# Kernel tuning notes

Hardware: AMD Instinct MI355X
Metric: run time of the kernel (lower is better)

Reference implementation:

```python
import jax, jax.numpy as jnp
import numpy as np

B, N, C, K = 8, 49104, 90, 1000  # batch, anchors, classes, pre-NMS top-k cap
NEG = -1e9


def _decode(reg, anc):
    # anchors ltrb -> cxcywh, apply reg, back to ltrb (matches decode_boxes)
    l, t, r, b = anc[..., 0], anc[..., 1], anc[..., 2], anc[..., 3]
    w_a, h_a = r - l, b - t
    cx_a, cy_a = l + w_a / 2, t + h_a / 2
    cx = cx_a + reg[..., 0] * w_a
    cy = cy_a + reg[..., 1] * h_a
    w = w_a * jnp.exp(reg[..., 2])
    h = h_a * jnp.exp(reg[..., 3])
    left, top = cx - w / 2, cy - h / 2
    return jnp.stack([left, top, left + w, top + h], -1)


def _iou(boxes):  # [K,4] -> [K,K]
    area = (boxes[:, 2] - boxes[:, 0]) * (boxes[:, 3] - boxes[:, 1])
    lt = jnp.maximum(boxes[:, None, :2], boxes[None, :, :2])
    rb = jnp.minimum(boxes[:, None, 2:], boxes[None, :, 2:])
    wh = jnp.clip(rb - lt, 0.0)
    inter = wh[..., 0] * wh[..., 1]
    return inter / (area[:, None] + area[None, :] - inter + 1e-9)


def _per_image(cls, reg, anchors, size, size_ori, score_thresh, nms_thresh):
    scores = jnp.max(cls, axis=-1)                       # [N]
    labels = jnp.argmax(cls, axis=-1).astype(jnp.int32)  # [N]
    valid = scores >= score_thresh
    boxes = _decode(reg, anchors)                        # [N,4] ltrb
    H = size[0].astype(jnp.float32)
    W = size[1].astype(jnp.float32)
    x = jnp.clip(boxes[..., 0::2], 0.0, W - 1.0)
    y = jnp.clip(boxes[..., 1::2], 0.0, H - 1.0)
    boxes = jnp.stack([x[..., 0], y[..., 0], x[..., 1], y[..., 1]], -1)
    # fixed-size substitute for nonzero(): take top-K by masked score
    ms = jnp.where(valid, scores, NEG)
    top_s, idx = jax.lax.top_k(ms, K)
    b, l, v = boxes[idx], labels[idx], valid[idx]        # [K,4],[K],[K]
    # batched_nms trick: offset boxes per class so classes never overlap
    off = l.astype(jnp.float32) * (jnp.maximum(W, H) + 1.0)
    iou = _iou(b + off[:, None])                         # [K,K]
    ar = jnp.arange(K)
    def body(i, supp):
        keep_i = v[i] & jnp.logical_not(supp[i])
        return supp | (keep_i & (iou[i] > nms_thresh) & (ar > i))
    supp = jax.lax.fori_loop(0, K, body, jnp.zeros((K,), bool))
    keep = v & jnp.logical_not(supp)
    scale = size_ori[0].astype(jnp.float32) / H
    b = b * scale
    out5 = jnp.concatenate(
        [jnp.where(keep[:, None], b, 0.0), jnp.where(keep, top_s, 0.0)[:, None]], -1)
    return out5, jnp.where(keep, l, -1), keep


def setup_inputs() -> dict:
    key = jax.random.key(0)
    k1, k2, k3, k4, k5, k6 = jax.random.split(key, 6)
    classifications = jax.random.uniform(k1, (B, N, C), dtype=jnp.float32)
    regressions = jax.random.normal(k2, (B, N, 4), dtype=jnp.float32) * 0.1
    cx = jax.random.uniform(k3, (N,), minval=0.0, maxval=512.0)
    cy = jax.random.uniform(k4, (N,), minval=0.0, maxval=512.0)
    w = jax.random.uniform(k5, (N,), minval=16.0, maxval=256.0)
    h = jax.random.uniform(k6, (N,), minval=16.0, maxval=256.0)
    anchors = jnp.stack([cx - w / 2, cy - h / 2, cx + w / 2, cy + h / 2], -1)
    return {
        'classifications': classifications,
        'regressions': regressions,
        'anchors': anchors,
        'image_sizes': jnp.full((B, 2), 512, dtype=jnp.int32),
        'image_sizes_ori': jnp.full((B, 2), 768, dtype=jnp.int32),
        'score_thresh': jnp.float32(0.999),
        'nms_thresh': jnp.float32(0.5),
    }


def reference(classifications, regressions, anchors, image_sizes, image_sizes_ori, score_thresh, nms_thresh):
    out5, labels, keep = jax.vmap(
        _per_image, in_axes=(0, 0, None, 0, 0, None, None))(
        classifications, regressions, anchors, image_sizes, image_sizes_ori,
        score_thresh, nms_thresh)
    return out5, labels, keep
```

## Files before the change

kernel.cpp:

```cpp
#include <hip/hip_runtime.h>
#include <stdint.h>

#define NB 8
#define NN 49104
#define NC 90
#define NK 1000
#define SA 192
#define NSEG 256
#define CAP2 8192
#define NB2 4352
#define NB2P 5120

typedef unsigned long long u64;

__global__ __launch_bounds__(768) void k_score(const float* __restrict__ cls,
                                               const float* __restrict__ thr_p,
                                               u64* __restrict__ cseg,
                                               unsigned* __restrict__ segcnt) {
  __shared__ __align__(16) float lds[SA * NC];
  __shared__ unsigned scnt;
  int b = blockIdx.y;
  int blk = blockIdx.x;
  int t0 = blk * SA;
  int tid = threadIdx.x;
  int lane = tid & 63;
  if (tid == 0) scnt = 0u;
  int acnt = NN - t0; if (acnt > SA) acnt = SA;
  const float4* src = (const float4*)(cls + ((size_t)b * NN + t0) * NC);
  float4* dst = (float4*)lds;
  int elems4 = acnt * NC / 4;
  for (int t = tid; t < elems4; t += 768) dst[t] = src[t];
  __syncthreads();
  int a = tid >> 2, q = tid & 3;
  float best = -1e30f; int bc = 0;
  if (a < acnt) {
    for (int c = q; c < NC; c += 4) {
      float v = lds[a * NC + c];
      if (v > best) { best = v; bc = c; }
    }
    float ov; int oc;
    ov = __shfl_xor(best, 1); oc = __shfl_xor(bc, 1);
    if (ov > best || (ov == best && oc < bc)) { best = ov; bc = oc; }
    ov = __shfl_xor(best, 2); oc = __shfl_xor(bc, 2);
    if (ov > best || (ov == best && oc < bc)) { best = ov; bc = oc; }
  }
  bool valid = (q == 0) && (a < acnt) && (best >= *thr_p);
  u64 key = 0ULL;
  if (valid) {
    unsigned idx = (unsigned)(t0 + a);
    key = ((u64)__float_as_uint(best) << 32) |
          ((u64)(0xFFFFu - idx) << 16) | (u64)(unsigned)bc;
  }
  __syncthreads();
  u64* kbuf = (u64*)lds;
  u64 m = __ballot(valid);
  if (m) {
    int leader = (int)__ffsll((unsigned long long)m) - 1;
    unsigned base = 0;
    if (lane == leader) base = atomicAdd(&scnt, (unsigned)__popcll(m));
    base = __shfl(base, leader);
    if (valid) {
      unsigned pos = base + (unsigned)__popcll(m & ((1ULL << lane) - 1ULL));
      kbuf[pos] = key;
    }
  }
  __syncthreads();
  unsigned cnt = scnt;
  u64* dseg = cseg + ((size_t)b * NSEG + blk) * SA;
  for (unsigned t = tid; t < cnt; t += 768) dseg[t] = kbuf[t];
  if (tid == 0) segcnt[b * NSEG + blk] = cnt;
}

__device__ __forceinline__ void decode_box(const float4 rg, const float4 an,
                                           float W, float H, float* out) {
#pragma clang fp contract(off)
  float l = an.x, t = an.y, r = an.z, bo = an.w;
  float wa = r - l, ha = bo - t;
  float cxa = l + wa * 0.5f, cya = t + ha * 0.5f;
  float cx = cxa + rg.x * wa;
  float cy = cya + rg.y * ha;
  float w = wa * expf(rg.z);
  float h = ha * expf(rg.w);
  float left = cx - w * 0.5f, top = cy - h * 0.5f;
  float right = left + w, botm = top + h;
  out[0] = fminf(fmaxf(left, 0.f), W - 1.f);
  out[1] = fminf(fmaxf(top, 0.f), H - 1.f);
  out[2] = fminf(fmaxf(right, 0.f), W - 1.f);
  out[3] = fminf(fmaxf(botm, 0.f), H - 1.f);
}

__global__ __launch_bounds__(1024) void k_worker(
    const u64* __restrict__ cseg, const unsigned* __restrict__ segcnt,
    const float* __restrict__ regs, const float* __restrict__ anch,
    const int* __restrict__ isz, const int* __restrict__ iszo,
    const float* __restrict__ nthr_p, float* __restrict__ out) {
#pragma clang fp contract(off)
  __shared__ __align__(16) char S[151552];
  __shared__ unsigned wsum[16];
  __shared__ unsigned segc[NSEG];
  __shared__ unsigned sofsL[NSEG + 1];
  __shared__ unsigned wcar[4];
  __shared__ int lcnt[NC];
  __shared__ int lofs[NC + 1];

  u64* cand = (u64*)S;
  u64* outk = (u64*)(S + 65536);
  unsigned* hist = (unsigned*)(S + 131072);

  int tid = threadIdx.x;
  int lane = tid & 63, wid = tid >> 6;
  int b = blockIdx.x;

  for (int i = tid; i < NB2P; i += 1024) hist[i] = 0u;
  if (tid < NSEG) {
    unsigned c = segcnt[b * NSEG + tid]; if (c > SA) c = SA;
    segc[tid] = c;
  }
  __syncthreads();

  unsigned vv = 0;
  if (tid < NSEG) {
    vv = segc[tid];
    for (int d = 1; d < 64; d <<= 1) {
      unsigned o = __shfl_up(vv, d);
      if (lane >= d) vv += o;
    }
    if (lane == 63) wcar[wid] = vv;
  }
  __syncthreads();
  if (tid < NSEG) {
    unsigned add = 0;
    for (int w = 0; w < wid; w++) add += wcar[w];
    sofsL[tid] = add + vv - segc[tid];
    if (tid == NSEG - 1) sofsL[NSEG] = add + vv;
  }
  __syncthreads();
  unsigned total = sofsL[NSEG]; if (total > CAP2) total = CAP2;

  {
    int s = tid >> 2, sub = tid & 3;
    unsigned c = segc[s], o = sofsL[s];
    const u64* srcp = cseg + ((size_t)b * NSEG + s) * SA;
    for (unsigned j = sub; j < c; j += 4) {
      u64 key = srcp[j];
      unsigned pos = o + j;
      if (pos < CAP2) {
        cand[pos] = key;
        unsigned bin = (0x3F800000u - (unsigned)(key >> 32) - 1u) >> 2;
        if (bin >= NB2) bin = NB2 - 1;
        atomicAdd(&hist[bin], 1u);
      }
    }
  }
  __syncthreads();

  int base5 = tid * 5;
  unsigned mysum = 0;
#pragma unroll
  for (int i = 0; i < 5; i++) mysum += hist[base5 + i];
  unsigned v = mysum;
  for (int d = 1; d < 64; d <<= 1) {
    unsigned o = __shfl_up(v, d);
    if (lane >= d) v += o;
  }
  if (lane == 63) wsum[wid] = v;
  __syncthreads();
  if (tid == 0) {
    unsigned acc = 0;
    for (int w2 = 0; w2 < 16; w2++) { unsigned c = wsum[w2]; wsum[w2] = acc; acc += c; }
  }
  __syncthreads();
  unsigned running = wsum[wid] + v - mysum;
#pragma unroll
  for (int i = 0; i < 5; i++) {
    unsigned c = hist[base5 + i];
    hist[base5 + i] = running;
    running += c;
  }
  __syncthreads();

  for (unsigned p = tid; p < total; p += 1024) {
    u64 key = cand[p];
    unsigned bin = (0x3F800000u - (unsigned)(key >> 32) - 1u) >> 2;
    if (bin >= NB2) bin = NB2 - 1;
    unsigned pos = atomicAdd(&hist[bin], 1u);
    if (pos < CAP2) outk[pos] = key;
  }
  __syncthreads();

  for (int bin = tid; bin < NB2; bin += 1024) {
    unsigned hi = hist[bin];
    unsigned lo = bin ? hist[bin - 1] : 0u;
    if (hi > CAP2) hi = CAP2;
    if (lo > CAP2) lo = CAP2;
    if (hi > lo + 1) {
      for (unsigned i2 = lo + 1; i2 < hi; i2++) {
        u64 kx = outk[i2];
        int j = (int)i2 - 1;
        while (j >= (int)lo && outk[j] < kx) { outk[j + 1] = outk[j]; j--; }
        outk[j + 1] = kx;
      }
    }
  }
  __syncthreads();

  int n = (int)total; if (n > NK) n = NK;
  float4* bo = (float4*)S;
  unsigned short* llab = (unsigned short*)(S + 16000);
  unsigned short* sidx = (unsigned short*)(S + 18000);
  unsigned char* live = (unsigned char*)(S + 20000);
  u64* clsbits = (u64*)(S + 21008);
  u64* nmsmask = (u64*)(S + 32536);

  float H = (float)isz[b * 2 + 0];
  float W = (float)isz[b * 2 + 1];
  float scale = (float)iszo[b * 2 + 0] / H;
  float offmul = fmaxf(W, H) + 1.0f;
  for (int i = tid; i < NC * 16; i += 1024) clsbits[i] = 0ULL;
  for (int k = tid; k < n; k += 1024) {
    u64 key = outk[k];
    float sc = __uint_as_float((unsigned)(key >> 32));
    unsigned idx = 0xFFFFu - (unsigned)((key >> 16) & 0xFFFFull);
    int lab = (int)(key & 0xFFFFull);
    float raw[4];
    float4 rg = ((const float4*)regs)[(size_t)b * NN + idx];
    float4 an = ((const float4*)anch)[idx];
    decode_box(rg, an, W, H, raw);
    float off = (float)lab * offmul;
    bo[k] = make_float4(raw[0] + off, raw[1] + off, raw[2] + off, raw[3] + off);
    llab[k] = (unsigned short)lab;
    live[k] = 1;
    int g = b * NK + k;
    float* o5 = out + (size_t)g * 5;
    o5[0] = raw[0] * scale; o5[1] = raw[1] * scale;
    o5[2] = raw[2] * scale; o5[3] = raw[3] * scale;
    o5[4] = sc;
    out[(size_t)NB * NK * 5 + g] = (float)lab;
  }
  __syncthreads();

  for (int k = tid; k < n; k += 1024)
    atomicOr(&clsbits[(int)llab[k] * 16 + (k >> 6)], 1ULL << (k & 63));
  __syncthreads();

  if (tid < NC) {
    unsigned cnt = 0;
#pragma unroll
    for (int w = 0; w < 16; w++) cnt += (unsigned)__popcll(clsbits[tid * 16 + w]);
    lcnt[tid] = (int)cnt;
  }
  __syncthreads();
  if (tid == 0) {
    int acc = 0;
    for (int c = 0; c < NC; c++) { lofs[c] = acc; acc += lcnt[c]; }
    lofs[NC] = acc;
  }
  __syncthreads();

  for (int k = tid; k < n; k += 1024) {
    int lab = (int)llab[k];
    const u64* cb = &clsbits[lab * 16];
    int w0 = k >> 6;
    unsigned pos = 0;
    for (int w = 0; w < w0; w++) pos += (unsigned)__popcll(cb[w]);
    pos += (unsigned)__popcll(cb[w0] & ((1ULL << (k & 63)) - 1ULL));
    sidx[lofs[lab] + pos] = (unsigned short)k;
  }
  __syncthreads();

  float thr = *nthr_p;
  for (int p = tid; p < n; p += 1024) {
    int ki = (int)sidx[p];
    int lab = (int)llab[ki];
    int s = lofs[lab], e = lofs[lab + 1];
    int r = p - s;
    if (r < 64) {
      u64 mask = 0ULL;
      float4 Bb = bo[ki];
      float x0 = Bb.x, y0 = Bb.y, x1 = Bb.z, y1 = Bb.w;
      float ai = (x1 - x0) * (y1 - y0);
      int qe = e; if (qe > s + 64) qe = s + 64;
      for (int q = p + 1; q < qe; q++) {
        int kj = (int)sidx[q];
        float4 Cc = bo[kj];
        float aj = (Cc.z - Cc.x) * (Cc.w - Cc.y);
        float ltx = fmaxf(x0, Cc.x), lty = fmaxf(y0, Cc.y);
        float rbx = fminf(x1, Cc.z), rby = fminf(y1, Cc.w);
        float ww = fmaxf(rbx - ltx, 0.f), hh = fmaxf(rby - lty, 0.f);
        float inter = ww * hh;
        float den = ((ai + aj) - inter) + 1e-9f;
        float iou = inter / den;
        if (iou > thr) mask |= 1ULL << (q - s);
      }
      nmsmask[lab * 64 + r] = mask;
    }
  }
  __syncthreads();

  if (tid < NC) {
    int s = lofs[tid], e = lofs[tid + 1], m = e - s;
    if (m <= 64) {
      u64 rem = 0ULL;
      for (int r = 0; r < m; r++)
        if (!((rem >> r) & 1ULL)) rem |= nmsmask[tid * 64 + r];
      for (int r = 0; r < m; r++)
        live[(int)sidx[s + r]] = (unsigned char)(1ULL ^ ((rem >> r) & 1ULL));
    } else {
      for (int r = 0; r < m; r++) live[(int)sidx[s + r]] = 1;
      for (int i = s; i < e; i++) {
        int ki = (int)sidx[i];
        if (!live[ki]) continue;
        float4 Bb = bo[ki];
        float x0 = Bb.x, y0 = Bb.y, x1 = Bb.z, y1 = Bb.w;
        float ai = (x1 - x0) * (y1 - y0);
        for (int j = i + 1; j < e; j++) {
          int kj = (int)sidx[j];
          if (!live[kj]) continue;
          float4 Cc = bo[kj];
          float aj = (Cc.z - Cc.x) * (Cc.w - Cc.y);
          float ltx = fmaxf(x0, Cc.x), lty = fmaxf(y0, Cc.y);
          float rbx = fminf(x1, Cc.z), rby = fminf(y1, Cc.w);
          float ww = fmaxf(rbx - ltx, 0.f), hh = fmaxf(rby - lty, 0.f);
          float inter = ww * hh;
          float den = ((ai + aj) - inter) + 1e-9f;
          float iou = inter / den;
          if (iou > thr) live[kj] = 0;
        }
      }
    }
  }
  __syncthreads();

  for (int k = tid; k < NK; k += 1024) {
    int g = b * NK + k;
    int keep = (k < n) ? (int)live[k] : 0;
    if (keep) {
      out[(size_t)NB * NK * 6 + g] = 1.0f;
    } else {
      float* o5 = out + (size_t)g * 5;
      o5[0] = 0.f; o5[1] = 0.f; o5[2] = 0.f; o5[3] = 0.f; o5[4] = 0.f;
      out[(size_t)NB * NK * 5 + g] = -1.0f;
      out[(size_t)NB * NK * 6 + g] = 0.0f;
    }
  }
}

extern "C" void kernel_launch(void* const* d_in, const int* in_sizes, int n_in,
                              void* d_out, int out_size, void* d_ws, size_t ws_size,
                              hipStream_t stream) {
  const float* cls = (const float*)d_in[0];
  const float* regs = (const float*)d_in[1];
  const float* anch = (const float*)d_in[2];
  const int* isz = (const int*)d_in[3];
  const int* iszo = (const int*)d_in[4];
  const float* sthr = (const float*)d_in[5];
  const float* nthr = (const float*)d_in[6];
  float* out = (float*)d_out;

  char* p = (char*)d_ws;
  auto alloc = [&](size_t bytes) {
    char* r = p;
    p += (bytes + 255) & ~(size_t)255;
    return r;
  };
  u64* cseg = (u64*)alloc((size_t)NB * NSEG * SA * 8);
  unsigned* segcnt = (unsigned*)alloc((size_t)NB * NSEG * 4);

  hipLaunchKernelGGL(k_score, dim3(NSEG, NB), dim3(768), 0, stream,
                     cls, sthr, cseg, segcnt);
  hipLaunchKernelGGL(k_worker, dim3(NB), dim3(1024), 0, stream,
                     cseg, segcnt, regs, anch, isz, iszo, nthr, out);
}
```

Before: 55.59 us.

## Fuse score and worker kernels into one persistent launch with atomic completion counters

```diff
diff --git a/kernel.cpp b/kernel.cpp
--- a/kernel.cpp
+++ b/kernel.cpp
@@ -7,68 +7,25 @@
 #define NK 1000
 #define SA 192
 #define NSEG 256
-#define CAP2 8192
+#define NTH 768
+#define CAP 6912
 #define NB2 4352
-#define NB2P 5120
+#define HISTN 5376
+#define NWORK 8
 
 typedef unsigned long long u64;
 
-__global__ __launch_bounds__(768) void k_score(const float* __restrict__ cls,
-                                               const float* __restrict__ thr_p,
-                                               u64* __restrict__ cseg,
-                                               unsigned* __restrict__ segcnt) {
-  __shared__ __align__(16) float lds[SA * NC];
-  __shared__ unsigned scnt;
-  int b = blockIdx.y;
-  int blk = blockIdx.x;
-  int t0 = blk * SA;
-  int tid = threadIdx.x;
-  int lane = tid & 63;
-  if (tid == 0) scnt = 0u;
-  int acnt = NN - t0; if (acnt > SA) acnt = SA;
-  const float4* src = (const float4*)(cls + ((size_t)b * NN + t0) * NC);
-  float4* dst = (float4*)lds;
-  int elems4 = acnt * NC / 4;
-  for (int t = tid; t < elems4; t += 768) dst[t] = src[t];
-  __syncthreads();
-  int a = tid >> 2, q = tid & 3;
-  float best = -1e30f; int bc = 0;
-  if (a < acnt) {
-    for (int c = q; c < NC; c += 4) {
-      float v = lds[a * NC + c];
-      if (v > best) { best = v; bc = c; }
-    }
-    float ov; int oc;
-    ov = __shfl_xor(best, 1); oc = __shfl_xor(bc, 1);
-    if (ov > best || (ov == best && oc < bc)) { best = ov; bc = oc; }
-    ov = __shfl_xor(best, 2); oc = __shfl_xor(bc, 2);
-    if (ov > best || (ov == best && oc < bc)) { best = ov; bc = oc; }
-  }
-  bool valid = (q == 0) && (a < acnt) && (best >= *thr_p);
-  u64 key = 0ULL;
-  if (valid) {
-    unsigned idx = (unsigned)(t0 + a);
-    key = ((u64)__float_as_uint(best) << 32) |
-          ((u64)(0xFFFFu - idx) << 16) | (u64)(unsigned)bc;
-  }
-  __syncthreads();
-  u64* kbuf = (u64*)lds;
-  u64 m = __ballot(valid);
-  if (m) {
-    int leader = (int)__ffsll((unsigned long long)m) - 1;
-    unsigned base = 0;
-    if (lane == leader) base = atomicAdd(&scnt, (unsigned)__popcll(m));
-    base = __shfl(base, leader);
-    if (valid) {
-      unsigned pos = base + (unsigned)__popcll(m & ((1ULL << lane) - 1ULL));
-      kbuf[pos] = key;
-    }
-  }
-  __syncthreads();
-  unsigned cnt = scnt;
-  u64* dseg = cseg + ((size_t)b * NSEG + blk) * SA;
-  for (unsigned t = tid; t < cnt; t += 768) dseg[t] = kbuf[t];
-  if (tid == 0) segcnt[b * NSEG + blk] = cnt;
+__device__ __forceinline__ u64 aload64(const u64* p) {
+  return __hip_atomic_load(p, __ATOMIC_RELAXED, __HIP_MEMORY_SCOPE_AGENT);
+}
+__device__ __forceinline__ void astore64(u64* p, u64 v) {
+  __hip_atomic_store(p, v, __ATOMIC_RELAXED, __HIP_MEMORY_SCOPE_AGENT);
+}
+__device__ __forceinline__ unsigned aload32(const unsigned* p) {
+  return __hip_atomic_load(p, __ATOMIC_RELAXED, __HIP_MEMORY_SCOPE_AGENT);
+}
+__device__ __forceinline__ void astore32(unsigned* p, unsigned v) {
+  __hip_atomic_store(p, v, __ATOMIC_RELAXED, __HIP_MEMORY_SCOPE_AGENT);
 }
 
 __device__ __forceinline__ void decode_box(const float4 rg, const float4 an,
@@ -89,31 +46,100 @@
   out[3] = fminf(fmaxf(botm, 0.f), H - 1.f);
 }
 
-__global__ __launch_bounds__(1024) void k_worker(
-    const u64* __restrict__ cseg, const unsigned* __restrict__ segcnt,
-    const float* __restrict__ regs, const float* __restrict__ anch,
-    const int* __restrict__ isz, const int* __restrict__ iszo,
-    const float* __restrict__ nthr_p, float* __restrict__ out) {
+__global__ __launch_bounds__(NTH) void k_mega(
+    const float* __restrict__ cls, const float* __restrict__ regs,
+    const float* __restrict__ anch, const int* __restrict__ isz,
+    const int* __restrict__ iszo, const float* __restrict__ sthr_p,
+    const float* __restrict__ nthr_p, u64* __restrict__ cseg,
+    unsigned* __restrict__ segcnt, unsigned* __restrict__ done,
+    float* __restrict__ out) {
 #pragma clang fp contract(off)
-  __shared__ __align__(16) char S[151552];
-  __shared__ unsigned wsum[16];
+  __shared__ __align__(16) char S[76800];
+  __shared__ unsigned wsum[12];
   __shared__ unsigned segc[NSEG];
   __shared__ unsigned sofsL[NSEG + 1];
   __shared__ unsigned wcar[4];
   __shared__ int lcnt[NC];
   __shared__ int lofs[NC + 1];
-
-  u64* cand = (u64*)S;
-  u64* outk = (u64*)(S + 65536);
-  unsigned* hist = (unsigned*)(S + 131072);
+  __shared__ unsigned scnt;
 
   int tid = threadIdx.x;
+  int bid = blockIdx.x;
   int lane = tid & 63, wid = tid >> 6;
-  int b = blockIdx.x;
-
-  for (int i = tid; i < NB2P; i += 1024) hist[i] = 0u;
+
+  if (bid >= NWORK) {
+    int sbid = bid - NWORK;
+    int b = sbid >> 8, blk = sbid & 255;
+    int t0 = blk * SA;
+    float* lds = (float*)S;
+    if (tid == 0) scnt = 0u;
+    int acnt = NN - t0; if (acnt > SA) acnt = SA;
+    const float4* src = (const float4*)(cls + ((size_t)b * NN + t0) * NC);
+    float4* dst = (float4*)lds;
+    int elems4 = acnt * NC / 4;
+    for (int t = tid; t < elems4; t += NTH) dst[t] = src[t];
+    __syncthreads();
+    int a = tid >> 2, q = tid & 3;
+    float best = -1e30f; int bc = 0;
+    if (a < acnt) {
+      for (int c = q; c < NC; c += 4) {
+        float v = lds[a * NC + c];
+        if (v > best) { best = v; bc = c; }
+      }
+      float ov; int oc;
+      ov = __shfl_xor(best, 1); oc = __shfl_xor(bc, 1);
+      if (ov > best || (ov == best && oc < bc)) { best = ov; bc = oc; }
+      ov = __shfl_xor(best, 2); oc = __shfl_xor(bc, 2);
+      if (ov > best || (ov == best && oc < bc)) { best = ov; bc = oc; }
+    }
+    bool valid = (q == 0) && (a < acnt) && (best >= *sthr_p);
+    u64 key = 0ULL;
+    if (valid) {
+      unsigned idx = (unsigned)(t0 + a);
+      key = ((u64)__float_as_uint(best) << 32) |
+            ((u64)(0xFFFFu - idx) << 16) | (u64)(unsigned)bc;
+    }
+    __syncthreads();
+    u64* kbuf = (u64*)S;
+    u64 m = __ballot(valid);
+    if (m) {
+      int leader = (int)__ffsll((unsigned long long)m) - 1;
+      unsigned base = 0;
+      if (lane == leader) base = atomicAdd(&scnt, (unsigned)__popcll(m));
+      base = __shfl(base, leader);
+      if (valid) {
+        unsigned pos = base + (unsigned)__popcll(m & ((1ULL << lane) - 1ULL));
+        kbuf[pos] = key;
+      }
+    }
+    __syncthreads();
+    unsigned cnt = scnt;
+    u64* dseg = cseg + ((size_t)b * NSEG + blk) * SA;
+    for (unsigned t = tid; t < cnt; t += NTH) astore64(&dseg[t], kbuf[t]);
+    __syncthreads();
+    if (tid == 0) {
+      astore32(&segcnt[b * NSEG + blk], cnt);
+      asm volatile("s_waitcnt vmcnt(0)" ::: "memory");
+      __hip_atomic_fetch_add(&done[b], 1u, __ATOMIC_RELAXED,
+                             __HIP_MEMORY_SCOPE_AGENT);
+    }
+    return;
+  }
+
+  int b = bid;
+  u64* outk = (u64*)S;
+  unsigned* hist = (unsigned*)(S + 55296);
+
+  for (int i = tid; i < HISTN; i += NTH) hist[i] = 0u;
+  if (tid == 0) {
+    while (__hip_atomic_load(&done[b], __ATOMIC_RELAXED,
+                             __HIP_MEMORY_SCOPE_AGENT) < NSEG)
+      __builtin_amdgcn_s_sleep(2);
+  }
+  __syncthreads();
+
   if (tid < NSEG) {
-    unsigned c = segcnt[b * NSEG + tid]; if (c > SA) c = SA;
+    unsigned c = aload32(&segcnt[b * NSEG + tid]); if (c > SA) c = SA;
     segc[tid] = c;
   }
   __syncthreads();
@@ -135,17 +161,15 @@
     if (tid == NSEG - 1) sofsL[NSEG] = add + vv;
   }
   __syncthreads();
-  unsigned total = sofsL[NSEG]; if (total > CAP2) total = CAP2;
+  unsigned total = sofsL[NSEG]; if (total > CAP) total = CAP;
 
   {
-    int s = tid >> 2, sub = tid & 3;
+    int s = tid / 3, sub = tid - s * 3;
     unsigned c = segc[s], o = sofsL[s];
     const u64* srcp = cseg + ((size_t)b * NSEG + s) * SA;
-    for (unsigned j = sub; j < c; j += 4) {
-      u64 key = srcp[j];
-      unsigned pos = o + j;
-      if (pos < CAP2) {
-        cand[pos] = key;
+    for (unsigned j = sub; j < c; j += 3) {
+      if (o + j < CAP) {
+        u64 key = aload64(&srcp[j]);
         unsigned bin = (0x3F800000u - (unsigned)(key >> 32) - 1u) >> 2;
         if (bin >= NB2) bin = NB2 - 1;
         atomicAdd(&hist[bin], 1u);
@@ -154,10 +178,10 @@
   }
   __syncthreads();
 
-  int base5 = tid * 5;
+  int base7 = tid * 7;
   unsigned mysum = 0;
 #pragma unroll
-  for (int i = 0; i < 5; i++) mysum += hist[base5 + i];
+  for (int i = 0; i < 7; i++) mysum += hist[base7 + i];
   unsigned v = mysum;
   for (int d = 1; d < 64; d <<= 1) {
     unsigned o = __shfl_up(v, d);
@@ -167,32 +191,39 @@
   __syncthreads();
   if (tid == 0) {
     unsigned acc = 0;
-    for (int w2 = 0; w2 < 16; w2++) { unsigned c = wsum[w2]; wsum[w2] = acc; acc += c; }
+    for (int w2 = 0; w2 < 12; w2++) { unsigned c = wsum[w2]; wsum[w2] = acc; acc += c; }
   }
   __syncthreads();
   unsigned running = wsum[wid] + v - mysum;
 #pragma unroll
-  for (int i = 0; i < 5; i++) {
-    unsigned c = hist[base5 + i];
-    hist[base5 + i] = running;
+  for (int i = 0; i < 7; i++) {
+    unsigned c = hist[base7 + i];
+    hist[base7 + i] = running;
     running += c;
   }
   __syncthreads();
 
-  for (unsigned p = tid; p < total; p += 1024) {
-    u64 key = cand[p];
-    unsigned bin = (0x3F800000u - (unsigned)(key >> 32) - 1u) >> 2;
-    if (bin >= NB2) bin = NB2 - 1;
-    unsigned pos = atomicAdd(&hist[bin], 1u);
-    if (pos < CAP2) outk[pos] = key;
-  }
-  __syncthreads();
-
-  for (int bin = tid; bin < NB2; bin += 1024) {
+  {
+    int s = tid / 3, sub = tid - s * 3;
+    unsigned c = segc[s], o = sofsL[s];
+    const u64* srcp = cseg + ((size_t)b * NSEG + s) * SA;
+    for (unsigned j = sub; j < c; j += 3) {
+      if (o + j < CAP) {
+        u64 key = aload64(&srcp[j]);
+        unsigned bin = (0x3F800000u - (unsigned)(key >> 32) - 1u) >> 2;
+        if (bin >= NB2) bin = NB2 - 1;
+        unsigned pos = atomicAdd(&hist[bin], 1u);
+        if (pos < CAP) outk[pos] = key;
+      }
+    }
+  }
+  __syncthreads();
+
+  for (int bin = tid; bin < NB2; bin += NTH) {
     unsigned hi = hist[bin];
     unsigned lo = bin ? hist[bin - 1] : 0u;
-    if (hi > CAP2) hi = CAP2;
-    if (lo > CAP2) lo = CAP2;
+    if (hi > CAP) hi = CAP;
+    if (lo > CAP) lo = CAP;
     if (hi > lo + 1) {
       for (unsigned i2 = lo + 1; i2 < hi; i2++) {
         u64 kx = outk[i2];
@@ -205,19 +236,19 @@
   __syncthreads();
 
   int n = (int)total; if (n > NK) n = NK;
-  float4* bo = (float4*)S;
-  unsigned short* llab = (unsigned short*)(S + 16000);
-  unsigned short* sidx = (unsigned short*)(S + 18000);
-  unsigned char* live = (unsigned char*)(S + 20000);
-  u64* clsbits = (u64*)(S + 21008);
-  u64* nmsmask = (u64*)(S + 32536);
+  float4* bo = (float4*)(S + 8192);
+  unsigned short* llab = (unsigned short*)(S + 24192);
+  unsigned short* sidx = (unsigned short*)(S + 26192);
+  unsigned char* live = (unsigned char*)(S + 28192);
+  u64* clsbits = (u64*)(S + 29200);
+  u64* nmsmask = (u64*)(S + 40720);
 
   float H = (float)isz[b * 2 + 0];
   float W = (float)isz[b * 2 + 1];
   float scale = (float)iszo[b * 2 + 0] / H;
   float offmul = fmaxf(W, H) + 1.0f;
-  for (int i = tid; i < NC * 16; i += 1024) clsbits[i] = 0ULL;
-  for (int k = tid; k < n; k += 1024) {
+  for (int i = tid; i < NC * 16; i += NTH) clsbits[i] = 0ULL;
+  for (int k = tid; k < n; k += NTH) {
     u64 key = outk[k];
     float sc = __uint_as_float((unsigned)(key >> 32));
     unsigned idx = 0xFFFFu - (unsigned)((key >> 16) & 0xFFFFull);
@@ -239,7 +270,7 @@
   }
   __syncthreads();
 
-  for (int k = tid; k < n; k += 1024)
+  for (int k = tid; k < n; k += NTH)
     atomicOr(&clsbits[(int)llab[k] * 16 + (k >> 6)], 1ULL << (k & 63));
   __syncthreads();
 
@@ -257,7 +288,7 @@
   }
   __syncthreads();
 
-  for (int k = tid; k < n; k += 1024) {
+  for (int k = tid; k < n; k += NTH) {
     int lab = (int)llab[k];
     const u64* cb = &clsbits[lab * 16];
     int w0 = k >> 6;
@@ -269,17 +300,17 @@
   __syncthreads();
 
   float thr = *nthr_p;
-  for (int p = tid; p < n; p += 1024) {
+  for (int p = tid; p < n; p += NTH) {
     int ki = (int)sidx[p];
     int lab = (int)llab[ki];
     int s = lofs[lab], e = lofs[lab + 1];
     int r = p - s;
-    if (r < 64) {
+    if (r < 32) {
       u64 mask = 0ULL;
       float4 Bb = bo[ki];
       float x0 = Bb.x, y0 = Bb.y, x1 = Bb.z, y1 = Bb.w;
       float ai = (x1 - x0) * (y1 - y0);
-      int qe = e; if (qe > s + 64) qe = s + 64;
+      int qe = e; if (qe > s + 32) qe = s + 32;
       for (int q = p + 1; q < qe; q++) {
         int kj = (int)sidx[q];
         float4 Cc = bo[kj];
@@ -292,17 +323,17 @@
         float iou = inter / den;
         if (iou > thr) mask |= 1ULL << (q - s);
       }
-      nmsmask[lab * 64 + r] = mask;
+      nmsmask[lab * 32 + r] = mask;
     }
   }
   __syncthreads();
 
   if (tid < NC) {
     int s = lofs[tid], e = lofs[tid + 1], m = e - s;
-    if (m <= 64) {
+    if (m <= 32) {
       u64 rem = 0ULL;
       for (int r = 0; r < m; r++)
-        if (!((rem >> r) & 1ULL)) rem |= nmsmask[tid * 64 + r];
+        if (!((rem >> r) & 1ULL)) rem |= nmsmask[tid * 32 + r];
       for (int r = 0; r < m; r++)
         live[(int)sidx[s + r]] = (unsigned char)(1ULL ^ ((rem >> r) & 1ULL));
     } else {
@@ -331,7 +362,7 @@
   }
   __syncthreads();
 
-  for (int k = tid; k < NK; k += 1024) {
+  for (int k = tid; k < NK; k += NTH) {
     int g = b * NK + k;
     int keep = (k < n) ? (int)live[k] : 0;
     if (keep) {
@@ -365,9 +396,10 @@
   };
   u64* cseg = (u64*)alloc((size_t)NB * NSEG * SA * 8);
   unsigned* segcnt = (unsigned*)alloc((size_t)NB * NSEG * 4);
-
-  hipLaunchKernelGGL(k_score, dim3(NSEG, NB), dim3(768), 0, stream,
-                     cls, sthr, cseg, segcnt);
-  hipLaunchKernelGGL(k_worker, dim3(NB), dim3(1024), 0, stream,
-                     cseg, segcnt, regs, anch, isz, iszo, nthr, out);
-}
+  unsigned* done = (unsigned*)alloc((size_t)NB * 4);
+
+  hipMemsetAsync(done, 0, (size_t)NB * sizeof(unsigned), stream);
+  hipLaunchKernelGGL(k_mega, dim3(NWORK + NB * NSEG), dim3(NTH), 0, stream,
+                     cls, regs, anch, isz, iszo, sthr, nthr,
+                     cseg, segcnt, done, out);
+}
```

Measured after the change: 84.31 us. 1.52x slower.
